# Performance work log

Hardware: AMD Instinct MI355X
Metric: run time of the kernel (lower is better)

## Reference

```python
import jax, jax.numpy as jnp
import numpy as np

N = 100000   # node_num
E = 1000000  # edges per relation
DIN, DH, DOUT = 64, 32, 64  # in_dim, out_dim//2, out_dim
EPS = 1e-5


def setup_inputs() -> dict:
    key = jax.random.key(0)
    ks = jax.random.split(key, 32)
    def w(k, shape):
        fan_in = shape[0]
        return jax.random.normal(k, shape, dtype=jnp.float32) / np.sqrt(fan_in)
    inp = {}
    inp["init_emb"] = jax.random.normal(ks[0], (N, DIN), dtype=jnp.float32)
    inp["pos_edges"] = jax.random.randint(ks[1], (2, E), 0, N, dtype=jnp.int32)
    inp["neg_edges"] = jax.random.randint(ks[2], (2, E), 0, N, dtype=jnp.int32)
    # conv1: two relation layers + self-loop layer, 64 -> 32
    inp["c1_Wp"] = w(ks[3], (DIN, DH)); inp["c1_bp"] = jnp.zeros((DH,), jnp.float32)
    inp["c1_Wn"] = w(ks[4], (DIN, DH)); inp["c1_bn"] = jnp.zeros((DH,), jnp.float32)
    inp["c1_Ws"] = w(ks[5], (DIN, DH)); inp["c1_bs"] = jnp.zeros((DH,), jnp.float32)
    # conv2: 32 -> 32
    inp["c2_Wp"] = w(ks[6], (DH, DH)); inp["c2_bp"] = jnp.zeros((DH,), jnp.float32)
    inp["c2_Wn"] = w(ks[7], (DH, DH)); inp["c2_bn"] = jnp.zeros((DH,), jnp.float32)
    inp["c2_Ws"] = w(ks[8], (DH, DH)); inp["c2_bs"] = jnp.zeros((DH,), jnp.float32)
    # self.weight: Linear(32 -> 64)
    inp["w_W"] = w(ks[9], (DH, DOUT)); inp["w_b"] = jnp.zeros((DOUT,), jnp.float32)
    # readout MLP: Linear(64,64)+BN+ReLU, Linear(64,64)+BN+ReLU, Linear(64,1)
    inp["m1_W"] = w(ks[10], (DOUT, DOUT)); inp["m1_b"] = jnp.zeros((DOUT,), jnp.float32)
    inp["g1"] = jnp.ones((DOUT,), jnp.float32); inp["b1"] = jnp.zeros((DOUT,), jnp.float32)
    inp["m2_W"] = w(ks[11], (DOUT, DOUT)); inp["m2_b"] = jnp.zeros((DOUT,), jnp.float32)
    inp["g2"] = jnp.ones((DOUT,), jnp.float32); inp["b2"] = jnp.zeros((DOUT,), jnp.float32)
    inp["m3_W"] = w(ks[12], (DOUT, 1)); inp["m3_b"] = jnp.zeros((1,), jnp.float32)
    return inp


def _conv(x, pe, ne, Wp, bp, Wn, bn_, Ws, bs):
    # gather -> per-relation linear -> scatter_add, summed over 2 relations + self loop
    mp = x[pe[0]] @ Wp + bp                                  # [E, d_out]
    agg = jax.ops.segment_sum(mp, pe[1], num_segments=N)      # [N, d_out]
    mn = x[ne[0]] @ Wn + bn_
    agg = agg + jax.ops.segment_sum(mn, ne[1], num_segments=N)
    return agg + x @ Ws + bs


def _batchnorm(h, g, b):
    m = h.mean(axis=0)
    v = h.var(axis=0)
    return (h - m) * jax.lax.rsqrt(v + EPS) * g + b


def reference(init_emb, pos_edges, neg_edges,
              c1_Wp, c1_bp, c1_Wn, c1_bn, c1_Ws, c1_bs,
              c2_Wp, c2_bp, c2_Wn, c2_bn, c2_Ws, c2_bs,
              w_W, w_b, m1_W, m1_b, g1, b1, m2_W, m2_b, g2, b2, m3_W, m3_b):
    z = jnp.tanh(_conv(init_emb, pos_edges, neg_edges, c1_Wp, c1_bp, c1_Wn, c1_bn, c1_Ws, c1_bs))
    z = jnp.tanh(_conv(z, pos_edges, neg_edges, c2_Wp, c2_bp, c2_Wn, c2_bn, c2_Ws, c2_bs))
    z = jnp.tanh(z @ w_W + w_b)                               # [N, 64]
    h = jax.nn.relu(_batchnorm(z @ m1_W + m1_b, g1, b1))      # dropout p=0.2 disabled (eval)
    h = jax.nn.relu(_batchnorm(h @ m2_W + m2_b, g2, b2))
    prob = jax.nn.sigmoid(h @ m3_W + m3_b)                    # [N, 1]
    return (z, prob)
```

## Files before the change

kernel.cpp:

```cpp
#include <hip/hip_runtime.h>
#include <cstdint>
#include <cstddef>

#define NN 100000
#define EE 1000000
#define EPSF 1e-5f
#define NBUK 391
#define NBUK2 (2*NBUK)
#define NBLK 256
#define EPB 7813
#define GSB 782
#define GTILES ((NN + 63) / 64)
#define MLP_GRID 512
#define XFT (NN / 16)
#define XF_GRID 512

typedef __attribute__((ext_vector_type(8))) short bf16x8;
typedef __attribute__((ext_vector_type(4))) float f32x4;

__device__ __forceinline__ void fatomic(float* p, float v) { unsafeAtomicAdd(p, v); }

__device__ __forceinline__ short f2bf(float f) {
    unsigned u = __float_as_uint(f);
    u += 0x7FFF + ((u >> 16) & 1);
    return (short)(u >> 16);
}
__device__ __forceinline__ float bf2f(short s) {
    return __uint_as_float(((unsigned)(unsigned short)s) << 16);
}
__device__ __forceinline__ void split8(const float4 v0, const float4 v1, bf16x8& hi, bf16x8& lo) {
    float a[8] = {v0.x, v0.y, v0.z, v0.w, v1.x, v1.y, v1.z, v1.w};
    #pragma unroll
    for (int i = 0; i < 8; i++) {
        short h = f2bf(a[i]);
        hi[i] = h;
        lo[i] = f2bf(a[i] - bf2f(h));
    }
}
__device__ __forceinline__ int kmap(int kg, int i) {
    return (i < 4) ? kg * 4 + i : 16 + kg * 4 + (i - 4);
}

__device__ __forceinline__ void edge_of(const int* __restrict__ pe, const int* __restrict__ ne,
                                        int s, int& src, int& dst, int& bucket) {
    if (s < EE) { src = pe[s]; dst = pe[EE + s]; bucket = dst >> 8; }
    else        { src = ne[s - EE]; dst = ne[s]; bucket = NBUK + (dst >> 8); }
}

__global__ __launch_bounds__(256) void k_hist(const int* __restrict__ pe,
                                              const int* __restrict__ ne,
                                              int* __restrict__ hist) {
    __shared__ int lh[NBUK2];
    for (int i = threadIdx.x; i < NBUK2; i += 256) lh[i] = 0;
    __syncthreads();
    int start = blockIdx.x * EPB, end = min(start + EPB, 2 * EE);
    for (int s = start + threadIdx.x; s < end; s += 256) {
        int src, dst, bucket;
        edge_of(pe, ne, s, src, dst, bucket);
        atomicAdd(&lh[bucket], 1);
    }
    __syncthreads();
    for (int i = threadIdx.x; i < NBUK2; i += 256)
        hist[i * NBLK + blockIdx.x] = lh[i];
}

__global__ __launch_bounds__(256) void k_gscan1(const int* __restrict__ in,
                                                int* __restrict__ out,
                                                int* __restrict__ partials) {
    int i = blockIdx.x * 256 + threadIdx.x;
    int v = in[i];
    __shared__ int s[256];
    s[threadIdx.x] = v;
    __syncthreads();
    for (int off = 1; off < 256; off <<= 1) {
        int u = (threadIdx.x >= off) ? s[threadIdx.x - off] : 0;
        __syncthreads();
        s[threadIdx.x] += u;
        __syncthreads();
    }
    out[i] = s[threadIdx.x] - v;
    if (threadIdx.x == 255) partials[blockIdx.x] = s[255];
}

__global__ __launch_bounds__(1024) void k_gscan2(int* __restrict__ partials) {
    __shared__ int s[1024];
    int v = (threadIdx.x < GSB) ? partials[threadIdx.x] : 0;
    s[threadIdx.x] = v;
    __syncthreads();
    for (int off = 1; off < 1024; off <<= 1) {
        int u = (threadIdx.x >= off) ? s[threadIdx.x - off] : 0;
        __syncthreads();
        s[threadIdx.x] += u;
        __syncthreads();
    }
    if (threadIdx.x < GSB) partials[threadIdx.x] = s[threadIdx.x] - v;
}

__global__ __launch_bounds__(256) void k_gscan3(const int* __restrict__ partials,
                                                int* __restrict__ out) {
    out[blockIdx.x * 256 + threadIdx.x] += partials[blockIdx.x];
}

__global__ __launch_bounds__(256) void k_binscatter(const int* __restrict__ pe,
                                                    const int* __restrict__ ne,
                                                    const int* __restrict__ soff,
                                                    unsigned long long* __restrict__ staging) {
    __shared__ int cur[NBUK2];
    for (int i = threadIdx.x; i < NBUK2; i += 256)
        cur[i] = soff[i * NBLK + blockIdx.x];
    __syncthreads();
    int start = blockIdx.x * EPB, end = min(start + EPB, 2 * EE);
    for (int s = start + threadIdx.x; s < end; s += 256) {
        int src, dst, bucket;
        edge_of(pe, ne, s, src, dst, bucket);
        int pos = atomicAdd(&cur[bucket], 1);
        staging[pos] = ((unsigned long long)(unsigned)dst << 32) | (unsigned)src;
    }
}

__global__ __launch_bounds__(256) void k_local(const unsigned long long* __restrict__ staging,
                                               const int* __restrict__ soff,
                                               int* __restrict__ rpP,
                                               int* __restrict__ rpN,
                                               int* __restrict__ csrAll) {
    int bucket = blockIdx.x;
    int rel = bucket >= NBUK;
    int nodeBase = (bucket - rel * NBUK) << 8;
    int bstart = soff[bucket * NBLK];
    int bend = (bucket == NBUK2 - 1) ? 2 * EE : soff[(bucket + 1) * NBLK];
    int tid = threadIdx.x;
    __shared__ int deg[256], sc[256];
    deg[tid] = 0;
    __syncthreads();
    for (int i = bstart + tid; i < bend; i += 256) {
        int d = (int)(staging[i] >> 32) & 255;
        atomicAdd(&deg[d], 1);
    }
    __syncthreads();
    int dv = deg[tid];
    sc[tid] = dv;
    __syncthreads();
    for (int off = 1; off < 256; off <<= 1) {
        int u = (tid >= off) ? sc[tid - off] : 0;
        __syncthreads();
        sc[tid] += u;
        __syncthreads();
    }
    int lrp = sc[tid] - dv;
    int nCount = min(256, NN - nodeBase);
    int relbase = rel ? EE : 0;
    if (tid < nCount) (rel ? rpN : rpP)[nodeBase + tid] = bstart - relbase + lrp;
    if (bucket == NBUK - 1 && tid == 0) rpP[NN] = EE;
    if (bucket == NBUK2 - 1 && tid == 0) rpN[NN] = EE;
    deg[tid] = lrp;
    __syncthreads();
    for (int i = bstart + tid; i < bend; i += 256) {
        unsigned long long v = staging[i];
        int d = (int)(v >> 32) & 255;
        int src = (int)(v & 0xffffffffu);
        int slot = atomicAdd(&deg[d], 1);
        csrAll[bstart + slot] = src;
    }
}

__global__ __launch_bounds__(192) __attribute__((amdgpu_waves_per_eu(2, 4)))
void k_xf1(const float* __restrict__ x,
           const float* __restrict__ Wp,
           const float* __restrict__ Wn,
           const float* __restrict__ Ws,
           float* __restrict__ xp,
           float* __restrict__ xn,
           float* __restrict__ xs) {
    int tid = threadIdx.x;
    int wvm = tid >> 6;
    int l = tid & 63;
    int r16 = l & 15, kg = l >> 4;
    const float* W = (wvm == 0) ? Wp : (wvm == 1) ? Wn : Ws;
    float* outm = (wvm == 0) ? xp : (wvm == 1) ? xn : xs;

    bf16x8 bh[2][2], bl[2][2];
    #pragma unroll
    for (int ct = 0; ct < 2; ct++)
        #pragma unroll
        for (int h = 0; h < 2; h++)
            #pragma unroll
            for (int i = 0; i < 8; i++) {
                int k = h * 32 + kmap(kg, i);
                float w = W[k * 32 + ct * 16 + r16];
                short hi = f2bf(w);
                bh[ct][h][i] = hi;
                bl[ct][h][i] = f2bf(w - bf2f(hi));
            }

    for (int tile = blockIdx.x; tile < XFT; tile += XF_GRID) {
        int rbase = tile * 16;
        int arow = rbase + r16;
        bf16x8 ah[2], al[2];
        #pragma unroll
        for (int h = 0; h < 2; h++) {
            int k0 = h * 32 + kg * 4;
            int k1 = h * 32 + 16 + kg * 4;
            float4 v0 = *(const float4*)&x[(size_t)arow * 64 + k0];
            float4 v1 = *(const float4*)&x[(size_t)arow * 64 + k1];
            split8(v0, v1, ah[h], al[h]);
        }
        f32x4 acc[2];
        #pragma unroll
        for (int ct = 0; ct < 2; ct++) { acc[ct][0] = 0.f; acc[ct][1] = 0.f; acc[ct][2] = 0.f; acc[ct][3] = 0.f; }
        #pragma unroll
        for (int h = 0; h < 2; h++)
            #pragma unroll
            for (int ct = 0; ct < 2; ct++) {
                acc[ct] = __builtin_amdgcn_mfma_f32_16x16x32_bf16(ah[h], bh[ct][h], acc[ct], 0, 0, 0);
                acc[ct] = __builtin_amdgcn_mfma_f32_16x16x32_bf16(al[h], bh[ct][h], acc[ct], 0, 0, 0);
                acc[ct] = __builtin_amdgcn_mfma_f32_16x16x32_bf16(ah[h], bl[ct][h], acc[ct], 0, 0, 0);
            }
        #pragma unroll
        for (int ct = 0; ct < 2; ct++)
            #pragma unroll
            for (int i = 0; i < 4; i++)
                outm[(size_t)(rbase + kg * 4 + i) * 32 + ct * 16 + r16] = acc[ct][i];
    }
}

__global__ __launch_bounds__(192) __attribute__((amdgpu_waves_per_eu(2, 4)))
void k_xf2(const float* __restrict__ z,
           const float* __restrict__ Wp,
           const float* __restrict__ Wn,
           const float* __restrict__ Ws,
           float* __restrict__ xp,
           float* __restrict__ xn,
           float* __restrict__ xs) {
    int tid = threadIdx.x;
    int wvm = tid >> 6;
    int l = tid & 63;
    int r16 = l & 15, kg = l >> 4;
    const float* W = (wvm == 0) ? Wp : (wvm == 1) ? Wn : Ws;
    float* outm = (wvm == 0) ? xp : (wvm == 1) ? xn : xs;

    bf16x8 bh[2], bl[2];
    #pragma unroll
    for (int ct = 0; ct < 2; ct++)
        #pragma unroll
        for (int i = 0; i < 8; i++) {
            int k = kmap(kg, i);
            float w = W[k * 32 + ct * 16 + r16];
            short hi = f2bf(w);
            bh[ct][i] = hi;
            bl[ct][i] = f2bf(w - bf2f(hi));
        }

    for (int tile = blockIdx.x; tile < XFT; tile += XF_GRID) {
        int rbase = tile * 16;
        int arow = rbase + r16;
        float4 v0 = *(const float4*)&z[(size_t)arow * 32 + kg * 4];
        float4 v1 = *(const float4*)&z[(size_t)arow * 32 + 16 + kg * 4];
        bf16x8 ah, al;
        split8(v0, v1, ah, al);
        f32x4 acc[2];
        #pragma unroll
        for (int ct = 0; ct < 2; ct++) { acc[ct][0] = 0.f; acc[ct][1] = 0.f; acc[ct][2] = 0.f; acc[ct][3] = 0.f; }
        #pragma unroll
        for (int ct = 0; ct < 2; ct++) {
            acc[ct] = __builtin_amdgcn_mfma_f32_16x16x32_bf16(ah, bh[ct], acc[ct], 0, 0, 0);
            acc[ct] = __builtin_amdgcn_mfma_f32_16x16x32_bf16(al, bh[ct], acc[ct], 0, 0, 0);
            acc[ct] = __builtin_amdgcn_mfma_f32_16x16x32_bf16(ah, bl[ct], acc[ct], 0, 0, 0);
        }
        #pragma unroll
        for (int ct = 0; ct < 2; ct++)
            #pragma unroll
            for (int i = 0; i < 4; i++)
                outm[(size_t)(rbase + kg * 4 + i) * 32 + ct * 16 + r16] = acc[ct][i];
    }
}

__device__ __forceinline__ float pull_rel(const float* __restrict__ xsrc,
                                          const int* __restrict__ csr,
                                          int b0, int b1, int j, float acc) {
    for (int base = b0; base < b1; base += 32) {
        int rem = b1 - base;
        int cnt = min(rem, 32);
        int idx = (j < rem) ? csr[base + j] : 0;
        int i = 0;
        for (; i + 4 <= cnt; i += 4) {
            int s0 = __shfl(idx, i, 32);
            int s1 = __shfl(idx, i + 1, 32);
            int s2 = __shfl(idx, i + 2, 32);
            int s3 = __shfl(idx, i + 3, 32);
            float v0 = xsrc[(size_t)s0 * 32 + j];
            float v1 = xsrc[(size_t)s1 * 32 + j];
            float v2 = xsrc[(size_t)s2 * 32 + j];
            float v3 = xsrc[(size_t)s3 * 32 + j];
            acc += v0; acc += v1; acc += v2; acc += v3;
        }
        for (; i < cnt; i++) {
            int s = __shfl(idx, i, 32);
            acc += xsrc[(size_t)s * 32 + j];
        }
    }
    return acc;
}

__global__ __launch_bounds__(256) void k_pull(const float* __restrict__ xp,
                                              const float* __restrict__ xn,
                                              const float* __restrict__ xs,
                                              const int* __restrict__ rpP,
                                              const int* __restrict__ csrP,
                                              const int* __restrict__ rpN,
                                              const int* __restrict__ csrN,
                                              const float* __restrict__ bp,
                                              const float* __restrict__ bn,
                                              const float* __restrict__ bs,
                                              float* __restrict__ out) {
    int j = threadIdx.x & 31;
    int hw = (blockIdx.x * 256 + threadIdx.x) >> 5;
    const int nhw = (2048 * 256) >> 5;
    float bpj = bp[j], bnj = bn[j], bsj = bs[j];
    for (int n = hw; n < NN; n += nhw) {
        int p0 = rpP[n], p1 = rpP[n + 1];
        int n0 = rpN[n], n1 = rpN[n + 1];
        float acc = xs[(size_t)n * 32 + j] + bsj
                  + (float)(p1 - p0) * bpj + (float)(n1 - n0) * bnj;
        acc = pull_rel(xp, csrP, p0, p1, j, acc);
        acc = pull_rel(xn, csrN, n0, n1, j, acc);
        out[(size_t)n * 32 + j] = tanhf(acc);
    }
}

__global__ __launch_bounds__(256) __attribute__((amdgpu_waves_per_eu(2, 4)))
void k_wlin(const float* __restrict__ z2,
            const float* __restrict__ Wl,
            const float* __restrict__ bl,
            float* __restrict__ z) {
    __shared__ float sx[64 * 32];
    int base = blockIdx.x * 64;
    int tid = threadIdx.x;
    int lane = tid & 63;
    int wv = tid >> 6;
    {
        int row = tid >> 2, c4 = tid & 3;
        int n = base + row;
        #pragma unroll
        for (int m = 0; m < 2; m++) {
            int f = c4 + 4 * m;
            float4 v = (n < NN) ? *(const float4*)&z2[(size_t)n * 32 + f * 4]
                                : make_float4(0.f, 0.f, 0.f, 0.f);
            *(float4*)&sx[row * 32 + f * 4] = v;
        }
    }
    float wl[32];
    #pragma unroll
    for (int k = 0; k < 32; k++) wl[k] = Wl[k * 64 + lane];
    float blj = bl[lane];
    __syncthreads();
    #pragma unroll 1
    for (int i = 0; i < 16; i++) {
        int nl = i * 4 + wv;
        int n = base + nl;
        float a0 = 0.f, a1c = 0.f, a2 = 0.f, a3 = 0.f;
        #pragma unroll
        for (int q = 0; q < 8; q++) {
            float4 xv = *(const float4*)&sx[nl * 32 + q * 4];
            a0 += xv.x * wl[q * 4 + 0];
            a1c += xv.y * wl[q * 4 + 1];
            a2 += xv.z * wl[q * 4 + 2];
            a3 += xv.w * wl[q * 4 + 3];
        }
        if (n < NN) z[(size_t)n * 64 + lane] = tanhf(blj + ((a0 + a1c) + (a2 + a3)));
    }
}

__global__ __launch_bounds__(256) __attribute__((amdgpu_waves_per_eu(2, 4)))
void k_mlp(const float* __restrict__ in,
           const float* __restrict__ a1,
           const float* __restrict__ c1,
           int doBN,
           const float* __restrict__ W,
           const float* __restrict__ b,
           float* __restrict__ out,
           float* __restrict__ colsum,
           float* __restrict__ colsq) {
    __shared__ float scol[64], ssq[64];
    int tid = threadIdx.x;
    if (tid < 64) { scol[tid] = 0.f; ssq[tid] = 0.f; }
    int wv = tid >> 6;
    int l = tid & 63;
    int r16 = l & 15, kg = l >> 4;

    bf16x8 bf[4][2];
    #pragma unroll
    for (int ct = 0; ct < 4; ct++)
        #pragma unroll
        for (int h = 0; h < 2; h++)
            #pragma unroll
            for (int i = 0; i < 8; i++) {
                int k = h * 32 + kmap(kg, i);
                bf[ct][h][i] = f2bf(W[k * 64 + ct * 16 + r16]);
            }
    float bj[4];
    #pragma unroll
    for (int ct = 0; ct < 4; ct++) bj[ct] = b[ct * 16 + r16];

    float av0[2][4], cv0[2][4], av1[2][4], cv1[2][4];
    #pragma unroll
    for (int h = 0; h < 2; h++) {
        int k0 = h * 32 + kg * 4;
        int k1 = h * 32 + 16 + kg * 4;
        #pragma unroll
        for (int i = 0; i < 4; i++) {
            av0[h][i] = doBN ? a1[k0 + i] : 1.f;
            cv0[h][i] = doBN ? c1[k0 + i] : 0.f;
            av1[h][i] = doBN ? a1[k1 + i] : 1.f;
            cv1[h][i] = doBN ? c1[k1 + i] : 0.f;
        }
    }

    float lsum[4] = {0.f, 0.f, 0.f, 0.f}, lsq[4] = {0.f, 0.f, 0.f, 0.f};

    for (int tile = blockIdx.x; tile < GTILES; tile += MLP_GRID) {
        int base = tile * 64;
        int arow = base + wv * 16 + r16;
        bool rv = arow < NN;
        bf16x8 af[2];
        #pragma unroll
        for (int h = 0; h < 2; h++) {
            int k0 = h * 32 + kg * 4;
            int k1 = h * 32 + 16 + kg * 4;
            float4 v0 = rv ? *(const float4*)&in[(size_t)arow * 64 + k0]
                           : make_float4(0.f, 0.f, 0.f, 0.f);
            float4 v1 = rv ? *(const float4*)&in[(size_t)arow * 64 + k1]
                           : make_float4(0.f, 0.f, 0.f, 0.f);
            if (doBN) {
                v0.x = fmaxf(v0.x * av0[h][0] + cv0[h][0], 0.f);
                v0.y = fmaxf(v0.y * av0[h][1] + cv0[h][1], 0.f);
                v0.z = fmaxf(v0.z * av0[h][2] + cv0[h][2], 0.f);
                v0.w = fmaxf(v0.w * av0[h][3] + cv0[h][3], 0.f);
                v1.x = fmaxf(v1.x * av1[h][0] + cv1[h][0], 0.f);
                v1.y = fmaxf(v1.y * av1[h][1] + cv1[h][1], 0.f);
                v1.z = fmaxf(v1.z * av1[h][2] + cv1[h][2], 0.f);
                v1.w = fmaxf(v1.w * av1[h][3] + cv1[h][3], 0.f);
            }
            af[h][0] = f2bf(v0.x); af[h][1] = f2bf(v0.y);
            af[h][2] = f2bf(v0.z); af[h][3] = f2bf(v0.w);
            af[h][4] = f2bf(v1.x); af[h][5] = f2bf(v1.y);
            af[h][6] = f2bf(v1.z); af[h][7] = f2bf(v1.w);
        }

        f32x4 acc[4];
        #pragma unroll
        for (int ct = 0; ct < 4; ct++) { acc[ct][0] = 0.f; acc[ct][1] = 0.f; acc[ct][2] = 0.f; acc[ct][3] = 0.f; }
        #pragma unroll
        for (int h = 0; h < 2; h++)
            #pragma unroll
            for (int ct = 0; ct < 4; ct++)
                acc[ct] = __builtin_amdgcn_mfma_f32_16x16x32_bf16(af[h], bf[ct][h], acc[ct], 0, 0, 0);

        #pragma unroll
        for (int ct = 0; ct < 4; ct++) {
            int col = ct * 16 + r16;
            #pragma unroll
            for (int i = 0; i < 4; i++) {
                int orow = base + wv * 16 + kg * 4 + i;
                if (orow < NN) {
                    float s = acc[ct][i] + bj[ct];
                    out[(size_t)orow * 64 + col] = s;
                    lsum[ct] += s; lsq[ct] += s * s;
                }
            }
        }
    }

    __syncthreads();
    #pragma unroll
    for (int ct = 0; ct < 4; ct++) {
        atomicAdd(&scol[ct * 16 + r16], lsum[ct]);
        atomicAdd(&ssq[ct * 16 + r16], lsq[ct]);
    }
    __syncthreads();
    if (tid < 64) {
        fatomic(&colsum[tid], scol[tid]);
        fatomic(&colsq[tid], ssq[tid]);
    }
}

__global__ void k_bnstats(const float* __restrict__ colsum, const float* __restrict__ colsq,
                          const float* __restrict__ g, const float* __restrict__ beta,
                          float* __restrict__ a, float* __restrict__ c) {
    int j = threadIdx.x;
    if (j < 64) {
        float m = colsum[j] * (1.f / NN);
        float v = colsq[j] * (1.f / NN) - m * m;
        float aj = g[j] * rsqrtf(v + EPSF);
        a[j] = aj;
        c[j] = beta[j] - m * aj;
    }
}

__global__ __launch_bounds__(256) void k_mlp3(const float* __restrict__ t2,
                                              const float* __restrict__ a2,
                                              const float* __restrict__ c2,
                                              const float* __restrict__ W3,
                                              const float* __restrict__ b3,
                                              float* __restrict__ prob) {
    int j = threadIdx.x & 63;
    int r = threadIdx.x >> 6;
    float aj = a2[j], cj = c2[j], wj = W3[j], bb = b3[0];
    for (int n = blockIdx.x * 4 + r; n < NN; n += 2048 * 4) {
        float h = fmaxf(t2[(size_t)n * 64 + j] * aj + cj, 0.f) * wj;
        #pragma unroll
        for (int off = 32; off > 0; off >>= 1) h += __shfl_xor(h, off, 64);
        if (j == 0) prob[n] = 1.f / (1.f + expf(-(h + bb)));
    }
}

extern "C" void kernel_launch(void* const* d_in, const int* in_sizes, int n_in,
                              void* d_out, int out_size, void* d_ws, size_t ws_size,
                              hipStream_t stream) {
    const float* init_emb = (const float*)d_in[0];
    const int* pe = (const int*)d_in[1];
    const int* ne = (const int*)d_in[2];
    const float* c1_Wp = (const float*)d_in[3];  const float* c1_bp = (const float*)d_in[4];
    const float* c1_Wn = (const float*)d_in[5];  const float* c1_bn = (const float*)d_in[6];
    const float* c1_Ws = (const float*)d_in[7];  const float* c1_bs = (const float*)d_in[8];
    const float* c2_Wp = (const float*)d_in[9];  const float* c2_bp = (const float*)d_in[10];
    const float* c2_Wn = (const float*)d_in[11]; const float* c2_bn = (const float*)d_in[12];
    const float* c2_Ws = (const float*)d_in[13]; const float* c2_bs = (const float*)d_in[14];
    const float* w_W = (const float*)d_in[15];   const float* w_b = (const float*)d_in[16];
    const float* m1_W = (const float*)d_in[17];  const float* m1_b = (const float*)d_in[18];
    const float* g1 = (const float*)d_in[19];    const float* b1 = (const float*)d_in[20];
    const float* m2_W = (const float*)d_in[21];  const float* m2_b = (const float*)d_in[22];
    const float* g2 = (const float*)d_in[23];    const float* b2 = (const float*)d_in[24];
    const float* m3_W = (const float*)d_in[25];  const float* m3_b = (const float*)d_in[26];

    size_t off = 0;
    auto alloc = [&](size_t bytes) -> void* {
        void* r = (char*)d_ws + off;
        off += (bytes + 255) & ~(size_t)255;
        return r;
    };
    float* sums = (float*)alloc(256 * 4);
    size_t zero_bytes = off;
    size_t csr_region = off;
    int*   hist = (int*)alloc((size_t)NBUK2 * NBLK * 4);
    int*   soff = (int*)alloc((size_t)NBUK2 * NBLK * 4);
    int*   part = (int*)alloc((size_t)1024 * 4);
    unsigned long long* staging = (unsigned long long*)alloc((size_t)2 * EE * 8);
    int*   csrAll = (int*)alloc((size_t)2 * EE * 4);
    int*   rpP  = (int*)alloc((size_t)(NN + 1) * 4);
    int*   rpN  = (int*)alloc((size_t)(NN + 1) * 4);
    float* R1   = (float*)alloc((size_t)NN * 96 * 4);
    float* z1   = (float*)alloc((size_t)NN * 32 * 4);
    float* z2   = (float*)alloc((size_t)NN * 32 * 4);
    float* abc  = (float*)alloc(256 * 4);

    int* csrP = csrAll;
    int* csrN = csrAll + (size_t)EE;
    float* xp = R1;
    float* xn = R1 + (size_t)NN * 32;
    float* xs = R1 + (size_t)NN * 64;
    float* t1 = R1;
    float* t2 = (float*)((char*)d_ws + csr_region);

    float* z_out = (float*)d_out;
    float* prob  = (float*)d_out + (size_t)NN * 64;

    hipMemsetAsync(d_ws, 0, zero_bytes, stream);

    k_hist<<<NBLK, 256, 0, stream>>>(pe, ne, hist);
    k_gscan1<<<GSB, 256, 0, stream>>>(hist, soff, part);
    k_gscan2<<<1, 1024, 0, stream>>>(part);
    k_gscan3<<<GSB, 256, 0, stream>>>(part, soff);
    k_binscatter<<<NBLK, 256, 0, stream>>>(pe, ne, soff, staging);
    k_local<<<NBUK2, 256, 0, stream>>>(staging, soff, rpP, rpN, csrAll);

    k_xf1<<<XF_GRID, 192, 0, stream>>>(init_emb, c1_Wp, c1_Wn, c1_Ws, xp, xn, xs);
    k_pull<<<2048, 256, 0, stream>>>(xp, xn, xs, rpP, csrP, rpN, csrN, c1_bp, c1_bn, c1_bs, z1);
    k_xf2<<<XF_GRID, 192, 0, stream>>>(z1, c2_Wp, c2_Wn, c2_Ws, xp, xn, xs);
    k_pull<<<2048, 256, 0, stream>>>(xp, xn, xs, rpP, csrP, rpN, csrN, c2_bp, c2_bn, c2_bs, z2);
    k_wlin<<<GTILES, 256, 0, stream>>>(z2, w_W, w_b, z_out);
    k_mlp<<<MLP_GRID, 256, 0, stream>>>(z_out, nullptr, nullptr, 0, m1_W, m1_b, t1, sums + 0, sums + 64);
    k_bnstats<<<1, 64, 0, stream>>>(sums + 0, sums + 64, g1, b1, abc + 0, abc + 64);
    k_mlp<<<MLP_GRID, 256, 0, stream>>>(t1, abc + 0, abc + 64, 1, m2_W, m2_b, t2, sums + 128, sums + 192);
    k_bnstats<<<1, 64, 0, stream>>>(sums + 128, sums + 192, g2, b2, abc + 128, abc + 192);
    k_mlp3<<<2048, 256, 0, stream>>>(t2, abc + 128, abc + 192, m3_W, m3_b, prob);
}
```

Before: 268.5 us.

## Pack staging edges into 32 bits and move output linear to split-bf16 MFMA

Edge staging entries now pack the local destination (8 bits) and the source index (20 bits) into one 32-bit word instead of a 64-bit pair. This halves the staging write and read traffic in binscatter and the local CSR build. The final 32->64 linear is rewritten to use bf16 MFMA with a hi/lo split (three MFMAs per tile) over 16-row tiles and a grid-stride loop, replacing the scalar FMA version that staged rows in LDS. The split-bf16 product approximates fp32 accuracy, and the 20-bit source field relies on N being below 2^20.

```diff
diff --git a/kernel.cpp b/kernel.cpp
--- a/kernel.cpp
+++ b/kernel.cpp
@@ -104,7 +104,7 @@
 __global__ __launch_bounds__(256) void k_binscatter(const int* __restrict__ pe,
                                                     const int* __restrict__ ne,
                                                     const int* __restrict__ soff,
-                                                    unsigned long long* __restrict__ staging) {
+                                                    unsigned* __restrict__ staging) {
     __shared__ int cur[NBUK2];
     for (int i = threadIdx.x; i < NBUK2; i += 256)
         cur[i] = soff[i * NBLK + blockIdx.x];
@@ -114,11 +114,11 @@
         int src, dst, bucket;
         edge_of(pe, ne, s, src, dst, bucket);
         int pos = atomicAdd(&cur[bucket], 1);
-        staging[pos] = ((unsigned long long)(unsigned)dst << 32) | (unsigned)src;
-    }
-}
-
-__global__ __launch_bounds__(256) void k_local(const unsigned long long* __restrict__ staging,
+        staging[pos] = ((unsigned)(dst & 255) << 20) | (unsigned)src;
+    }
+}
+
+__global__ __launch_bounds__(256) void k_local(const unsigned* __restrict__ staging,
                                                const int* __restrict__ soff,
                                                int* __restrict__ rpP,
                                                int* __restrict__ rpN,
@@ -133,7 +133,7 @@
     deg[tid] = 0;
     __syncthreads();
     for (int i = bstart + tid; i < bend; i += 256) {
-        int d = (int)(staging[i] >> 32) & 255;
+        int d = (int)(staging[i] >> 20);
         atomicAdd(&deg[d], 1);
     }
     __syncthreads();
@@ -155,9 +155,9 @@
     deg[tid] = lrp;
     __syncthreads();
     for (int i = bstart + tid; i < bend; i += 256) {
-        unsigned long long v = staging[i];
-        int d = (int)(v >> 32) & 255;
-        int src = (int)(v & 0xffffffffu);
+        unsigned v = staging[i];
+        int d = (int)(v >> 20);
+        int src = (int)(v & 0xFFFFFu);
         int slot = atomicAdd(&deg[d], 1);
         csrAll[bstart + slot] = src;
     }
@@ -332,41 +332,47 @@
             const float* __restrict__ Wl,
             const float* __restrict__ bl,
             float* __restrict__ z) {
-    __shared__ float sx[64 * 32];
-    int base = blockIdx.x * 64;
     int tid = threadIdx.x;
-    int lane = tid & 63;
     int wv = tid >> 6;
-    {
-        int row = tid >> 2, c4 = tid & 3;
-        int n = base + row;
-        #pragma unroll
-        for (int m = 0; m < 2; m++) {
-            int f = c4 + 4 * m;
-            float4 v = (n < NN) ? *(const float4*)&z2[(size_t)n * 32 + f * 4]
-                                : make_float4(0.f, 0.f, 0.f, 0.f);
-            *(float4*)&sx[row * 32 + f * 4] = v;
-        }
-    }
-    float wl[32];
-    #pragma unroll
-    for (int k = 0; k < 32; k++) wl[k] = Wl[k * 64 + lane];
-    float blj = bl[lane];
-    __syncthreads();
-    #pragma unroll 1
-    for (int i = 0; i < 16; i++) {
-        int nl = i * 4 + wv;
-        int n = base + nl;
-        float a0 = 0.f, a1c = 0.f, a2 = 0.f, a3 = 0.f;
-        #pragma unroll
-        for (int q = 0; q < 8; q++) {
-            float4 xv = *(const float4*)&sx[nl * 32 + q * 4];
-            a0 += xv.x * wl[q * 4 + 0];
-            a1c += xv.y * wl[q * 4 + 1];
-            a2 += xv.z * wl[q * 4 + 2];
-            a3 += xv.w * wl[q * 4 + 3];
-        }
-        if (n < NN) z[(size_t)n * 64 + lane] = tanhf(blj + ((a0 + a1c) + (a2 + a3)));
+    int l = tid & 63;
+    int r16 = l & 15, kg = l >> 4;
+
+    bf16x8 bh[4], blo[4];
+    #pragma unroll
+    for (int ct = 0; ct < 4; ct++)
+        #pragma unroll
+        for (int i = 0; i < 8; i++) {
+            int k = kmap(kg, i);
+            float w = Wl[k * 64 + ct * 16 + r16];
+            short hi = f2bf(w);
+            bh[ct][i] = hi;
+            blo[ct][i] = f2bf(w - bf2f(hi));
+        }
+    float bj[4];
+    #pragma unroll
+    for (int ct = 0; ct < 4; ct++) bj[ct] = bl[ct * 16 + r16];
+
+    for (int tile = blockIdx.x * 4 + wv; tile < XFT; tile += XF_GRID * 4) {
+        int rbase = tile * 16;
+        int arow = rbase + r16;
+        float4 v0 = *(const float4*)&z2[(size_t)arow * 32 + kg * 4];
+        float4 v1 = *(const float4*)&z2[(size_t)arow * 32 + 16 + kg * 4];
+        bf16x8 ah, al;
+        split8(v0, v1, ah, al);
+        f32x4 acc[4];
+        #pragma unroll
+        for (int ct = 0; ct < 4; ct++) { acc[ct][0] = 0.f; acc[ct][1] = 0.f; acc[ct][2] = 0.f; acc[ct][3] = 0.f; }
+        #pragma unroll
+        for (int ct = 0; ct < 4; ct++) {
+            acc[ct] = __builtin_amdgcn_mfma_f32_16x16x32_bf16(ah, bh[ct], acc[ct], 0, 0, 0);
+            acc[ct] = __builtin_amdgcn_mfma_f32_16x16x32_bf16(al, bh[ct], acc[ct], 0, 0, 0);
+            acc[ct] = __builtin_amdgcn_mfma_f32_16x16x32_bf16(ah, blo[ct], acc[ct], 0, 0, 0);
+        }
+        #pragma unroll
+        for (int ct = 0; ct < 4; ct++)
+            #pragma unroll
+            for (int i = 0; i < 4; i++)
+                z[(size_t)(rbase + kg * 4 + i) * 64 + ct * 16 + r16] = tanhf(acc[ct][i] + bj[ct]);
     }
 }
 
@@ -544,7 +550,7 @@
     int*   hist = (int*)alloc((size_t)NBUK2 * NBLK * 4);
     int*   soff = (int*)alloc((size_t)NBUK2 * NBLK * 4);
     int*   part = (int*)alloc((size_t)1024 * 4);
-    unsigned long long* staging = (unsigned long long*)alloc((size_t)2 * EE * 8);
+    unsigned* staging = (unsigned*)alloc((size_t)2 * EE * 8);
     int*   csrAll = (int*)alloc((size_t)2 * EE * 4);
     int*   rpP  = (int*)alloc((size_t)(NN + 1) * 4);
     int*   rpN  = (int*)alloc((size_t)(NN + 1) * 4);
@@ -577,7 +583,7 @@
     k_pull<<<2048, 256, 0, stream>>>(xp, xn, xs, rpP, csrP, rpN, csrN, c1_bp, c1_bn, c1_bs, z1);
     k_xf2<<<XF_GRID, 192, 0, stream>>>(z1, c2_Wp, c2_Wn, c2_Ws, xp, xn, xs);
     k_pull<<<2048, 256, 0, stream>>>(xp, xn, xs, rpP, csrP, rpN, csrN, c2_bp, c2_bn, c2_bs, z2);
-    k_wlin<<<GTILES, 256, 0, stream>>>(z2, w_W, w_b, z_out);
+    k_wlin<<<XF_GRID, 256, 0, stream>>>(z2, w_W, w_b, z_out);
     k_mlp<<<MLP_GRID, 256, 0, stream>>>(z_out, nullptr, nullptr, 0, m1_W, m1_b, t1, sums + 0, sums + 64);
     k_bnstats<<<1, 64, 0, stream>>>(sums + 0, sums + 64, g1, b1, abc + 0, abc + 64);
     k_mlp<<<MLP_GRID, 256, 0, stream>>>(t1, abc + 0, abc + 64, 1, m2_W, m2_b, t2, sums + 128, sums + 192);
```

After: 261.3 us. 2.7% less time.
